# Optimization experiments

Measured on AMD Instinct MI355X. Metric: run time of the kernel, lower is better.

Reference implementation:

```python
import jax, jax.numpy as jnp
import numpy as np

N = 100000   # nodes
E = 1600000  # edges
D = 128      # in_dim == hidden_dim
EL = 100000  # label edges for decode


def setup_inputs() -> dict:
    key = jax.random.key(0)
    k1, k2, k3, k4, k5 = jax.random.split(key, 5)
    x = jax.random.normal(k1, (N, D), dtype=jnp.float32)
    edge_index = jax.random.randint(k2, (2, E), 0, N, dtype=jnp.int64)
    edge_label_index = jax.random.randint(k3, (2, EL), 0, N, dtype=jnp.int64)
    # Glorot-ish init for GCN weights
    scale = 1.0 / np.sqrt(D)
    W1 = jax.random.normal(k4, (D, D), dtype=jnp.float32) * scale
    W2 = jax.random.normal(k5, (D, D), dtype=jnp.float32) * scale
    b1 = jnp.zeros((D,), dtype=jnp.float32)
    b2 = jnp.zeros((D,), dtype=jnp.float32)
    return {"x": x, "edge_index": edge_index, "edge_label_index": edge_label_index,
            "W1": W1, "b1": b1, "W2": W2, "b2": b2}


def gcn_conv(x, src, dst, W, b, num_nodes):
    # PyG GCNConv: add self-loops, symmetric D^-1/2 A D^-1/2 normalization
    loop = jnp.arange(num_nodes, dtype=src.dtype)
    s = jnp.concatenate([src, loop])
    d = jnp.concatenate([dst, loop])
    deg = jax.ops.segment_sum(jnp.ones(d.shape, dtype=x.dtype), d, num_segments=num_nodes)
    dinv = jnp.where(deg > 0, jax.lax.rsqrt(jnp.maximum(deg, 1.0)), 0.0)
    norm = dinv[s] * dinv[d]                      # [E+N]
    h = x @ W                                     # [N, H]
    msg = h[s] * norm[:, None]                    # gather + scale
    out = jax.ops.segment_sum(msg, d, num_segments=num_nodes)  # scatter-add
    return out + b


def reference(x, edge_index, edge_label_index, W1, b1, W2, b2):
    src, dst = edge_index[0], edge_index[1]
    z = jax.nn.relu(gcn_conv(x, src, dst, W1, b1, N))
    z = jax.nn.relu(gcn_conv(z, src, dst, W2, b2, N))
    # decode: edge-wise dot product
    s, d = edge_label_index[0], edge_label_index[1]
    return jnp.sum(z[s] * z[d], axis=-1)          # [EL]
```

## Files before the change

### kernel.cpp

```cpp
#include <hip/hip_runtime.h>
#include <hip/hip_bf16.h>
#include <hip/hip_fp16.h>


typedef _Float16 half8 __attribute__((ext_vector_type(8)));
typedef float floatx4 __attribute__((ext_vector_type(4)));

#define BK_SHIFT 8
#define BSC_EDGES 2048
#define SLAB_CAP 5120
#define WPAD 136

__global__ __launch_bounds__(128) void k_wprep(const float* __restrict__ W1,
                                               const float* __restrict__ W2,
                                               _Float16* __restrict__ WT1,
                                               _Float16* __restrict__ WT2,
                                               int* __restrict__ bfill) {
    int b = blockIdx.x;
    const float* W = (b < 128) ? W1 : W2;
    _Float16* WT = (b < 128) ? WT1 : WT2;
    int k = b & 127;
    int c = threadIdx.x;
    WT[c * 128 + k] = (_Float16)W[k * 128 + c];
    if (b < 4) bfill[b * 128 + c] = 0;
}

__global__ __launch_bounds__(256) void k_bscatter(const int* __restrict__ src,
                                                  const int* __restrict__ dst,
                                                  int* __restrict__ bfill,
                                                  int2* __restrict__ pairs,
                                                  int E, int nbk) {
    __shared__ int lcnt[1024];
    __shared__ int delta[1024];
    __shared__ int ssum[256];
    __shared__ int2 stage[BSC_EDGES];
    int tid = threadIdx.x;
    int e0 = blockIdx.x * BSC_EDGES;
    int nloc = E - e0; if (nloc > BSC_EDGES) nloc = BSC_EDGES;

    for (int b = tid; b < nbk; b += 256) lcnt[b] = 0;
    __syncthreads();

    int d[BSC_EDGES / 256], s[BSC_EDGES / 256];
#pragma unroll
    for (int k = 0; k < BSC_EDGES / 256; ++k) {
        int e = e0 + k * 256 + tid;
        if (e < E) {
            d[k] = dst[e];
            s[k] = src[e];
            atomicAdd(&lcnt[d[k] >> BK_SHIFT], 1);
        } else d[k] = -1;
    }
    __syncthreads();

    const int gpb = (nbk + 255) >> 8;
    int c[4], mysum = 0;
    for (int t = 0; t < gpb; ++t) {
        int b = tid * gpb + t;
        c[t] = (b < nbk) ? lcnt[b] : 0;
        mysum += c[t];
    }
    ssum[tid] = mysum;
    __syncthreads();
    for (int off = 1; off < 256; off <<= 1) {
        int t = (tid >= off) ? ssum[tid - off] : 0;
        __syncthreads();
        ssum[tid] += t;
        __syncthreads();
    }
    int base = ssum[tid] - mysum;
    for (int t = 0; t < gpb; ++t) {
        int b = tid * gpb + t;
        if (b < nbk) {
            int g = c[t] ? atomicAdd(&bfill[b], c[t]) : 0;
            delta[b] = b * SLAB_CAP + g - base;
            lcnt[b] = base;
            base += c[t];
        }
    }
    __syncthreads();

#pragma unroll
    for (int k = 0; k < BSC_EDGES / 256; ++k) {
        if (d[k] >= 0) {
            int b = d[k] >> BK_SHIFT;
            int lp = atomicAdd(&lcnt[b], 1);
            int2 p; p.x = s[k]; p.y = d[k];
            stage[lp] = p;
        }
    }
    __syncthreads();

    for (int j = tid; j < nloc; j += 256) {
        int2 p = stage[j];
        pairs[delta[p.y >> BK_SHIFT] + j] = p;
    }
}

__global__ __launch_bounds__(256) void k_csr(const int2* __restrict__ pairs,
                                             const int* __restrict__ bfill,
                                             int* __restrict__ row_start,
                                             int* __restrict__ cnt,
                                             float* __restrict__ dinv,
                                             int* __restrict__ srcs, int n) {
    __shared__ int lcnt[256];
    __shared__ int lpos[256];
    int tid = threadIdx.x;
    int b = blockIdx.x;
    lcnt[tid] = 0;
    __syncthreads();
    int beg = b * SLAB_CAP, end = beg + bfill[b];
    for (int i = beg + tid; i < end; i += 256)
        atomicAdd(&lcnt[pairs[i].y & 255], 1);
    __syncthreads();
    int c = lcnt[tid];
    lpos[tid] = c;
    __syncthreads();
    for (int off = 1; off < 256; off <<= 1) {
        int t = (tid >= off) ? lpos[tid - off] : 0;
        __syncthreads();
        lpos[tid] += t;
        __syncthreads();
    }
    int rs = beg + lpos[tid] - c;
    int v = (b << BK_SHIFT) + tid;
    if (v < n) {
        row_start[v] = rs;
        cnt[v] = c;
        dinv[v] = rsqrtf((float)c + 1.0f);
    }
    __syncthreads();
    lpos[tid] = rs;
    __syncthreads();
    for (int i = beg + tid; i < end; i += 256) {
        int2 p = pairs[i];
        int loc = atomicAdd(&lpos[p.y & 255], 1);
        srcs[loc] = p.x;
    }
}

template <typename AT>
__global__ __launch_bounds__(256) void k_gemm_mfma(const AT* __restrict__ X,
                                                   const _Float16* __restrict__ WT,
                                                   const float* __restrict__ dinv,
                                                   _Float16* __restrict__ G, int n) {
    __shared__ _Float16 Wl[128 * WPAD];
    int tid = threadIdx.x;
    {
        const half8* w8 = (const half8*)WT;
#pragma unroll
        for (int i = 0; i < 8; ++i) {
            int idx = i * 256 + tid;
            int r = idx >> 4, cc = idx & 15;
            *(half8*)(Wl + r * WPAD + cc * 8) = w8[idx];
        }
    }
    __syncthreads();

    auto loadA = [](const AT* p) -> half8 {
        if constexpr (sizeof(AT) == 4) {
            const float4* f = (const float4*)p;
            float4 f0 = f[0], f1 = f[1];
            half8 a;
            a[0] = (_Float16)f0.x; a[1] = (_Float16)f0.y;
            a[2] = (_Float16)f0.z; a[3] = (_Float16)f0.w;
            a[4] = (_Float16)f1.x; a[5] = (_Float16)f1.y;
            a[6] = (_Float16)f1.z; a[7] = (_Float16)f1.w;
            return a;
        } else {
            return *(const half8*)p;
        }
    };

    int wave = tid >> 6, lane = tid & 63;
    int q = lane >> 4, ln = lane & 15;
    int m0 = blockIdx.x * 128 + wave * 32;
    int mA0 = m0 + ln;      if (mA0 >= n) mA0 = n - 1;
    int mA1 = m0 + 16 + ln; if (mA1 >= n) mA1 = n - 1;
    const AT* xr0 = X + (size_t)mA0 * 128;
    const AT* xr1 = X + (size_t)mA1 * 128;

    floatx4 acc[2][8];
#pragma unroll
    for (int p = 0; p < 2; ++p)
#pragma unroll
        for (int t = 0; t < 8; ++t) acc[p][t] = (floatx4){0.f, 0.f, 0.f, 0.f};

#pragma unroll
    for (int kc = 0; kc < 128; kc += 32) {
        half8 a0 = loadA(xr0 + kc + q * 8);
        half8 a1 = loadA(xr1 + kc + q * 8);
#pragma unroll
        for (int t = 0; t < 8; ++t) {
            half8 b = *(const half8*)(Wl + (size_t)(t * 16 + ln) * WPAD + kc + q * 8);
            acc[0][t] = __builtin_amdgcn_mfma_f32_16x16x32_f16(a0, b, acc[0][t], 0, 0, 0);
            acc[1][t] = __builtin_amdgcn_mfma_f32_16x16x32_f16(a1, b, acc[1][t], 0, 0, 0);
        }
    }

#pragma unroll
    for (int p = 0; p < 2; ++p) {
#pragma unroll
        for (int r = 0; r < 4; ++r) {
            int row = m0 + p * 16 + q * 4 + r;
            if (row < n) {
                float dv = dinv[row];
                _Float16* grow = G + (size_t)row * 128 + ln;
#pragma unroll
                for (int t = 0; t < 8; ++t)
                    grow[t * 16] = (_Float16)(acc[p][t][r] * dv);
            }
        }
    }
}

__global__ __launch_bounds__(256) void k_gather_relu(const _Float16* __restrict__ G,
                                                     const int* __restrict__ srcs,
                                                     const int* __restrict__ row_start,
                                                     const int* __restrict__ cnt,
                                                     const float* __restrict__ dinv,
                                                     const float* __restrict__ bias,
                                                     _Float16* __restrict__ Z, int n) {
    int v = blockIdx.x * 16 + (threadIdx.x >> 4);
    int lane = threadIdx.x & 15;
    if (v >= n) return;
    const half8* G8 = (const half8*)G;

    half8 self = G8[(size_t)v * 16 + lane];
    float acc[8], acc2[8];
#pragma unroll
    for (int j = 0; j < 8; ++j) { acc[j] = (float)self[j]; acc2[j] = 0.f; }

    int beg = row_start[v], deg = cnt[v];
    int e = 0;
    for (; e + 3 < deg; e += 4) {
        int s0 = srcs[beg + e];
        int s1 = srcs[beg + e + 1];
        int s2 = srcs[beg + e + 2];
        int s3 = srcs[beg + e + 3];
        half8 t0 = G8[(size_t)s0 * 16 + lane];
        half8 t1 = G8[(size_t)s1 * 16 + lane];
        half8 t2 = G8[(size_t)s2 * 16 + lane];
        half8 t3 = G8[(size_t)s3 * 16 + lane];
#pragma unroll
        for (int j = 0; j < 8; ++j) {
            acc[j]  += (float)t0[j] + (float)t1[j];
            acc2[j] += (float)t2[j] + (float)t3[j];
        }
    }
    for (; e < deg; ++e) {
        int s0 = srcs[beg + e];
        half8 t0 = G8[(size_t)s0 * 16 + lane];
#pragma unroll
        for (int j = 0; j < 8; ++j) acc[j] += (float)t0[j];
    }

    float dv = dinv[v];
    const float4* b4 = (const float4*)bias;
    float4 bb0 = b4[lane * 2], bb1 = b4[lane * 2 + 1];
    float bf[8] = {bb0.x, bb0.y, bb0.z, bb0.w, bb1.x, bb1.y, bb1.z, bb1.w};
    half8 zo;
#pragma unroll
    for (int j = 0; j < 8; ++j) {
        float z = dv * (acc[j] + acc2[j]) + bf[j];
        zo[j] = (_Float16)fmaxf(z, 0.f);
    }
    ((half8*)Z)[(size_t)v * 16 + lane] = zo;
}

__global__ __launch_bounds__(256) void k_decode(const _Float16* __restrict__ Z,
                                                const int* __restrict__ eli,
                                                float* __restrict__ out, int el) {
    int sub = threadIdx.x >> 4, lane = threadIdx.x & 15;
    int e = blockIdx.x * 16 + sub;
    if (e >= el) return;
    int s = eli[e], d = eli[el + e];
    const half8* Z8 = (const half8*)Z;
    half8 a = Z8[(size_t)s * 16 + lane];
    half8 b = Z8[(size_t)d * 16 + lane];
    float dot = 0.f;
#pragma unroll
    for (int j = 0; j < 8; ++j) dot += (float)a[j] * (float)b[j];
#pragma unroll
    for (int off = 8; off; off >>= 1) dot += __shfl_down(dot, off, 16);
    if (lane == 0) out[e] = dot;
}

extern "C" void kernel_launch(void* const* d_in, const int* in_sizes, int n_in,
                              void* d_out, int out_size, void* d_ws, size_t ws_size,
                              hipStream_t stream) {
    const float* x  = (const float*)d_in[0];
    const int*  ei  = (const int*)d_in[1];
    const int*  eli = (const int*)d_in[2];
    const float* W1 = (const float*)d_in[3];
    const float* b1 = (const float*)d_in[4];
    const float* W2 = (const float*)d_in[5];
    const float* b2 = (const float*)d_in[6];
    float* out = (float*)d_out;

    const int N  = in_sizes[0] / 128;
    const int E  = in_sizes[1] / 2;
    const int EL = in_sizes[2] / 2;
    const int* src = ei;
    const int* dst = ei + E;
    const int NBK = (N + 255) >> BK_SHIFT;

    char* ws = (char*)d_ws;
    size_t off = 0;
    auto alloc = [&](size_t bytes) -> void* {
        void* p = ws + off;
        off += bytes;
        off = (off + 255) & ~(size_t)255;
        return p;
    };
    int*       cnt       = (int*)alloc((size_t)N * 4);
    int*       row_start = (int*)alloc((size_t)N * 4);
    float*     dinv      = (float*)alloc((size_t)N * 4);
    int*       bfill     = (int*)alloc(4096);
    _Float16*  WT1       = (_Float16*)alloc(128 * 128 * 2);
    _Float16*  WT2       = (_Float16*)alloc(128 * 128 * 2);
    int*       srcs      = (int*)alloc((size_t)NBK * SLAB_CAP * 4);
    int2*      pairs     = (int2*)alloc((size_t)NBK * SLAB_CAP * 8);
    _Float16*  buf0      = (_Float16*)alloc((size_t)N * 128 * 2);
    _Float16*  buf1      = (_Float16*)alloc((size_t)N * 128 * 2);

    k_wprep<<<256, 128, 0, stream>>>(W1, W2, WT1, WT2, bfill);

    k_bscatter<<<(E + BSC_EDGES - 1) / BSC_EDGES, 256, 0, stream>>>(src, dst, bfill, pairs, E, NBK);
    k_csr<<<NBK, 256, 0, stream>>>(pairs, bfill, row_start, cnt, dinv, srcs, N);

    k_gemm_mfma<float><<<(N + 127) / 128, 256, 0, stream>>>(x, WT1, dinv, buf0, N);
    k_gather_relu<<<(N + 15) / 16, 256, 0, stream>>>(buf0, srcs, row_start, cnt, dinv, b1, buf1, N);
    k_gemm_mfma<_Float16><<<(N + 127) / 128, 256, 0, stream>>>(buf1, WT2, dinv, buf0, N);
    k_gather_relu<<<(N + 15) / 16, 256, 0, stream>>>(buf0, srcs, row_start, cnt, dinv, b2, buf1, N);
    k_decode<<<(EL + 15) / 16, 256, 0, stream>>>(buf1, eli, out, EL);
}
```

Measured before the change: 307.7 us.

## Store node features as column-sliced planes to localize gather working set

```diff
diff --git a/kernel.cpp b/kernel.cpp
--- a/kernel.cpp
+++ b/kernel.cpp
@@ -10,6 +10,7 @@
 #define BSC_EDGES 2048
 #define SLAB_CAP 5120
 #define WPAD 136
+#define NSLICE 8
 
 __global__ __launch_bounds__(128) void k_wprep(const float* __restrict__ W1,
                                                const float* __restrict__ W2,
@@ -157,19 +158,17 @@
     }
     __syncthreads();
 
+    const size_t pl = (size_t)n * 16;
+
     auto loadA = [](const AT* p) -> half8 {
-        if constexpr (sizeof(AT) == 4) {
-            const float4* f = (const float4*)p;
-            float4 f0 = f[0], f1 = f[1];
-            half8 a;
-            a[0] = (_Float16)f0.x; a[1] = (_Float16)f0.y;
-            a[2] = (_Float16)f0.z; a[3] = (_Float16)f0.w;
-            a[4] = (_Float16)f1.x; a[5] = (_Float16)f1.y;
-            a[6] = (_Float16)f1.z; a[7] = (_Float16)f1.w;
-            return a;
-        } else {
-            return *(const half8*)p;
-        }
+        const float4* f = (const float4*)p;
+        float4 f0 = f[0], f1 = f[1];
+        half8 a;
+        a[0] = (_Float16)f0.x; a[1] = (_Float16)f0.y;
+        a[2] = (_Float16)f0.z; a[3] = (_Float16)f0.w;
+        a[4] = (_Float16)f1.x; a[5] = (_Float16)f1.y;
+        a[6] = (_Float16)f1.z; a[7] = (_Float16)f1.w;
+        return a;
     };
 
     int wave = tid >> 6, lane = tid & 63;
@@ -188,8 +187,16 @@
 
 #pragma unroll
     for (int kc = 0; kc < 128; kc += 32) {
-        half8 a0 = loadA(xr0 + kc + q * 8);
-        half8 a1 = loadA(xr1 + kc + q * 8);
+        half8 a0, a1;
+        if constexpr (sizeof(AT) == 4) {
+            a0 = loadA(xr0 + kc + q * 8);
+            a1 = loadA(xr1 + kc + q * 8);
+        } else {
+            int col0 = kc + q * 8;
+            const _Float16* base = (const _Float16*)X + (size_t)(col0 >> 4) * pl + (col0 & 15);
+            a0 = *(const half8*)(base + (size_t)mA0 * 16);
+            a1 = *(const half8*)(base + (size_t)mA1 * 16);
+        }
 #pragma unroll
         for (int t = 0; t < 8; ++t) {
             half8 b = *(const half8*)(Wl + (size_t)(t * 16 + ln) * WPAD + kc + q * 8);
@@ -205,10 +212,10 @@
             int row = m0 + p * 16 + q * 4 + r;
             if (row < n) {
                 float dv = dinv[row];
-                _Float16* grow = G + (size_t)row * 128 + ln;
+                _Float16* grow = G + (size_t)row * 16 + ln;
 #pragma unroll
                 for (int t = 0; t < 8; ++t)
-                    grow[t * 16] = (_Float16)(acc[p][t][r] * dv);
+                    grow[t * pl] = (_Float16)(acc[p][t][r] * dv);
             }
         }
     }
@@ -221,12 +228,14 @@
                                                      const float* __restrict__ dinv,
                                                      const float* __restrict__ bias,
                                                      _Float16* __restrict__ Z, int n) {
-    int v = blockIdx.x * 16 + (threadIdx.x >> 4);
-    int lane = threadIdx.x & 15;
+    int slice = blockIdx.x & 7;
+    int v = (blockIdx.x >> 3) * 128 + (threadIdx.x >> 1);
     if (v >= n) return;
-    const half8* G8 = (const half8*)G;
-
-    half8 self = G8[(size_t)v * 16 + lane];
+    int h = threadIdx.x & 1;
+    size_t pl8 = (size_t)n * 2;
+    const half8* Gp = (const half8*)G + (size_t)slice * pl8;
+
+    half8 self = Gp[(size_t)v * 2 + h];
     float acc[8], acc2[8];
 #pragma unroll
     for (int j = 0; j < 8; ++j) { acc[j] = (float)self[j]; acc2[j] = 0.f; }
@@ -234,14 +243,14 @@
     int beg = row_start[v], deg = cnt[v];
     int e = 0;
     for (; e + 3 < deg; e += 4) {
-        int s0 = srcs[beg + e];
-        int s1 = srcs[beg + e + 1];
-        int s2 = srcs[beg + e + 2];
-        int s3 = srcs[beg + e + 3];
-        half8 t0 = G8[(size_t)s0 * 16 + lane];
-        half8 t1 = G8[(size_t)s1 * 16 + lane];
-        half8 t2 = G8[(size_t)s2 * 16 + lane];
-        half8 t3 = G8[(size_t)s3 * 16 + lane];
+        int s0 = __builtin_nontemporal_load(srcs + beg + e);
+        int s1 = __builtin_nontemporal_load(srcs + beg + e + 1);
+        int s2 = __builtin_nontemporal_load(srcs + beg + e + 2);
+        int s3 = __builtin_nontemporal_load(srcs + beg + e + 3);
+        half8 t0 = Gp[(size_t)s0 * 2 + h];
+        half8 t1 = Gp[(size_t)s1 * 2 + h];
+        half8 t2 = Gp[(size_t)s2 * 2 + h];
+        half8 t3 = Gp[(size_t)s3 * 2 + h];
 #pragma unroll
         for (int j = 0; j < 8; ++j) {
             acc[j]  += (float)t0[j] + (float)t1[j];
@@ -249,15 +258,15 @@
         }
     }
     for (; e < deg; ++e) {
-        int s0 = srcs[beg + e];
-        half8 t0 = G8[(size_t)s0 * 16 + lane];
+        int s0 = __builtin_nontemporal_load(srcs + beg + e);
+        half8 t0 = Gp[(size_t)s0 * 2 + h];
 #pragma unroll
         for (int j = 0; j < 8; ++j) acc[j] += (float)t0[j];
     }
 
     float dv = dinv[v];
     const float4* b4 = (const float4*)bias;
-    float4 bb0 = b4[lane * 2], bb1 = b4[lane * 2 + 1];
+    float4 bb0 = b4[slice * 4 + h * 2], bb1 = b4[slice * 4 + h * 2 + 1];
     float bf[8] = {bb0.x, bb0.y, bb0.z, bb0.w, bb1.x, bb1.y, bb1.z, bb1.w};
     half8 zo;
 #pragma unroll
@@ -265,19 +274,21 @@
         float z = dv * (acc[j] + acc2[j]) + bf[j];
         zo[j] = (_Float16)fmaxf(z, 0.f);
     }
-    ((half8*)Z)[(size_t)v * 16 + lane] = zo;
+    ((half8*)Z)[(size_t)slice * pl8 + (size_t)v * 2 + h] = zo;
 }
 
 __global__ __launch_bounds__(256) void k_decode(const _Float16* __restrict__ Z,
                                                 const int* __restrict__ eli,
-                                                float* __restrict__ out, int el) {
+                                                float* __restrict__ out, int el, int n) {
     int sub = threadIdx.x >> 4, lane = threadIdx.x & 15;
     int e = blockIdx.x * 16 + sub;
     if (e >= el) return;
     int s = eli[e], d = eli[el + e];
-    const half8* Z8 = (const half8*)Z;
-    half8 a = Z8[(size_t)s * 16 + lane];
-    half8 b = Z8[(size_t)d * 16 + lane];
+    size_t pl8 = (size_t)n * 2;
+    const half8* Zp = (const half8*)Z + (size_t)(lane >> 1) * pl8;
+    int h = lane & 1;
+    half8 a = Zp[(size_t)s * 2 + h];
+    half8 b = Zp[(size_t)d * 2 + h];
     float dot = 0.f;
 #pragma unroll
     for (int j = 0; j < 8; ++j) dot += (float)a[j] * (float)b[j];
@@ -329,9 +340,10 @@
     k_bscatter<<<(E + BSC_EDGES - 1) / BSC_EDGES, 256, 0, stream>>>(src, dst, bfill, pairs, E, NBK);
     k_csr<<<NBK, 256, 0, stream>>>(pairs, bfill, row_start, cnt, dinv, srcs, N);
 
+    const int GRID_GATHER = ((N + 127) / 128) * NSLICE;
     k_gemm_mfma<float><<<(N + 127) / 128, 256, 0, stream>>>(x, WT1, dinv, buf0, N);
-    k_gather_relu<<<(N + 15) / 16, 256, 0, stream>>>(buf0, srcs, row_start, cnt, dinv, b1, buf1, N);
+    k_gather_relu<<<GRID_GATHER, 256, 0, stream>>>(buf0, srcs, row_start, cnt, dinv, b1, buf1, N);
     k_gemm_mfma<_Float16><<<(N + 127) / 128, 256, 0, stream>>>(buf1, WT2, dinv, buf0, N);
-    k_gather_relu<<<(N + 15) / 16, 256, 0, stream>>>(buf0, srcs, row_start, cnt, dinv, b2, buf1, N);
-    k_decode<<<(EL + 15) / 16, 256, 0, stream>>>(buf1, eli, out, EL);
-}
+    k_gather_relu<<<GRID_GATHER, 256, 0, stream>>>(buf0, srcs, row_start, cnt, dinv, b2, buf1, N);
+    k_decode<<<(EL + 15) / 16, 256, 0, stream>>>(buf1, eli, out, EL, N);
+}
```

New measurement: 464.1 us. 50.8% more time.

## Fuse CSR build with first GEMM and move source normalization into gather

Applied to the files above, without the earlier changes.

```diff
diff --git a/kernel.cpp b/kernel.cpp
--- a/kernel.cpp
+++ b/kernel.cpp
@@ -97,55 +97,58 @@
     }
 }
 
-__global__ __launch_bounds__(256) void k_csr(const int2* __restrict__ pairs,
-                                             const int* __restrict__ bfill,
-                                             int* __restrict__ row_start,
-                                             int* __restrict__ cnt,
-                                             float* __restrict__ dinv,
-                                             int* __restrict__ srcs, int n) {
-    __shared__ int lcnt[256];
-    __shared__ int lpos[256];
+template <typename AT>
+__global__ __launch_bounds__(256) void k_csr_gemm(const int2* __restrict__ pairs,
+                                                  const int* __restrict__ bfill,
+                                                  int* __restrict__ row_start,
+                                                  int* __restrict__ cnt,
+                                                  float* __restrict__ dinv,
+                                                  int* __restrict__ srcs,
+                                                  const AT* __restrict__ X,
+                                                  const _Float16* __restrict__ WT,
+                                                  _Float16* __restrict__ G,
+                                                  int n, int nbk) {
+    __shared__ __align__(16) char smem[128 * WPAD * 2];
     int tid = threadIdx.x;
-    int b = blockIdx.x;
-    lcnt[tid] = 0;
-    __syncthreads();
-    int beg = b * SLAB_CAP, end = beg + bfill[b];
-    for (int i = beg + tid; i < end; i += 256)
-        atomicAdd(&lcnt[pairs[i].y & 255], 1);
-    __syncthreads();
-    int c = lcnt[tid];
-    lpos[tid] = c;
-    __syncthreads();
-    for (int off = 1; off < 256; off <<= 1) {
-        int t = (tid >= off) ? lpos[tid - off] : 0;
-        __syncthreads();
-        lpos[tid] += t;
-        __syncthreads();
-    }
-    int rs = beg + lpos[tid] - c;
-    int v = (b << BK_SHIFT) + tid;
-    if (v < n) {
-        row_start[v] = rs;
-        cnt[v] = c;
-        dinv[v] = rsqrtf((float)c + 1.0f);
-    }
-    __syncthreads();
-    lpos[tid] = rs;
-    __syncthreads();
-    for (int i = beg + tid; i < end; i += 256) {
-        int2 p = pairs[i];
-        int loc = atomicAdd(&lpos[p.y & 255], 1);
-        srcs[loc] = p.x;
-    }
-}
-
-template <typename AT>
-__global__ __launch_bounds__(256) void k_gemm_mfma(const AT* __restrict__ X,
-                                                   const _Float16* __restrict__ WT,
-                                                   const float* __restrict__ dinv,
-                                                   _Float16* __restrict__ G, int n) {
-    __shared__ _Float16 Wl[128 * WPAD];
-    int tid = threadIdx.x;
+
+    if ((int)blockIdx.x < nbk) {
+        int* lcnt = (int*)smem;
+        int* lpos = lcnt + 256;
+        int b = blockIdx.x;
+        lcnt[tid] = 0;
+        __syncthreads();
+        int beg = b * SLAB_CAP, end = beg + bfill[b];
+        for (int i = beg + tid; i < end; i += 256)
+            atomicAdd(&lcnt[pairs[i].y & 255], 1);
+        __syncthreads();
+        int c = lcnt[tid];
+        lpos[tid] = c;
+        __syncthreads();
+        for (int off = 1; off < 256; off <<= 1) {
+            int t = (tid >= off) ? lpos[tid - off] : 0;
+            __syncthreads();
+            lpos[tid] += t;
+            __syncthreads();
+        }
+        int rs = beg + lpos[tid] - c;
+        int v = (b << BK_SHIFT) + tid;
+        if (v < n) {
+            row_start[v] = rs;
+            cnt[v] = c;
+            dinv[v] = rsqrtf((float)c + 1.0f);
+        }
+        __syncthreads();
+        lpos[tid] = rs;
+        __syncthreads();
+        for (int i = beg + tid; i < end; i += 256) {
+            int2 p = pairs[i];
+            int loc = atomicAdd(&lpos[p.y & 255], 1);
+            srcs[loc] = p.x;
+        }
+        return;
+    }
+
+    _Float16* Wl = (_Float16*)smem;
     {
         const half8* w8 = (const half8*)WT;
 #pragma unroll
@@ -172,6 +175,80 @@
         }
     };
 
+    int bid = blockIdx.x - nbk;
+    int wave = tid >> 6, lane = tid & 63;
+    int q = lane >> 4, ln = lane & 15;
+    int m0 = bid * 128 + wave * 32;
+    int mA0 = m0 + ln;      if (mA0 >= n) mA0 = n - 1;
+    int mA1 = m0 + 16 + ln; if (mA1 >= n) mA1 = n - 1;
+    const AT* xr0 = X + (size_t)mA0 * 128;
+    const AT* xr1 = X + (size_t)mA1 * 128;
+
+    floatx4 acc[2][8];
+#pragma unroll
+    for (int p = 0; p < 2; ++p)
+#pragma unroll
+        for (int t = 0; t < 8; ++t) acc[p][t] = (floatx4){0.f, 0.f, 0.f, 0.f};
+
+#pragma unroll
+    for (int kc = 0; kc < 128; kc += 32) {
+        half8 a0 = loadA(xr0 + kc + q * 8);
+        half8 a1 = loadA(xr1 + kc + q * 8);
+#pragma unroll
+        for (int t = 0; t < 8; ++t) {
+            half8 b = *(const half8*)(Wl + (size_t)(t * 16 + ln) * WPAD + kc + q * 8);
+            acc[0][t] = __builtin_amdgcn_mfma_f32_16x16x32_f16(a0, b, acc[0][t], 0, 0, 0);
+            acc[1][t] = __builtin_amdgcn_mfma_f32_16x16x32_f16(a1, b, acc[1][t], 0, 0, 0);
+        }
+    }
+
+#pragma unroll
+    for (int p = 0; p < 2; ++p) {
+#pragma unroll
+        for (int r = 0; r < 4; ++r) {
+            int row = m0 + p * 16 + q * 4 + r;
+            if (row < n) {
+                _Float16* grow = G + (size_t)row * 128 + ln;
+#pragma unroll
+                for (int t = 0; t < 8; ++t)
+                    grow[t * 16] = (_Float16)acc[p][t][r];
+            }
+        }
+    }
+}
+
+template <typename AT>
+__global__ __launch_bounds__(256) void k_gemm_mfma(const AT* __restrict__ X,
+                                                   const _Float16* __restrict__ WT,
+                                                   _Float16* __restrict__ G, int n) {
+    __shared__ _Float16 Wl[128 * WPAD];
+    int tid = threadIdx.x;
+    {
+        const half8* w8 = (const half8*)WT;
+#pragma unroll
+        for (int i = 0; i < 8; ++i) {
+            int idx = i * 256 + tid;
+            int r = idx >> 4, cc = idx & 15;
+            *(half8*)(Wl + r * WPAD + cc * 8) = w8[idx];
+        }
+    }
+    __syncthreads();
+
+    auto loadA = [](const AT* p) -> half8 {
+        if constexpr (sizeof(AT) == 4) {
+            const float4* f = (const float4*)p;
+            float4 f0 = f[0], f1 = f[1];
+            half8 a;
+            a[0] = (_Float16)f0.x; a[1] = (_Float16)f0.y;
+            a[2] = (_Float16)f0.z; a[3] = (_Float16)f0.w;
+            a[4] = (_Float16)f1.x; a[5] = (_Float16)f1.y;
+            a[6] = (_Float16)f1.z; a[7] = (_Float16)f1.w;
+            return a;
+        } else {
+            return *(const half8*)p;
+        }
+    };
+
     int wave = tid >> 6, lane = tid & 63;
     int q = lane >> 4, ln = lane & 15;
     int m0 = blockIdx.x * 128 + wave * 32;
@@ -204,11 +281,10 @@
         for (int r = 0; r < 4; ++r) {
             int row = m0 + p * 16 + q * 4 + r;
             if (row < n) {
-                float dv = dinv[row];
                 _Float16* grow = G + (size_t)row * 128 + ln;
 #pragma unroll
                 for (int t = 0; t < 8; ++t)
-                    grow[t * 16] = (_Float16)(acc[p][t][r] * dv);
+                    grow[t * 16] = (_Float16)acc[p][t][r];
             }
         }
     }
@@ -226,10 +302,11 @@
     if (v >= n) return;
     const half8* G8 = (const half8*)G;
 
+    float dv = dinv[v];
     half8 self = G8[(size_t)v * 16 + lane];
     float acc[8], acc2[8];
 #pragma unroll
-    for (int j = 0; j < 8; ++j) { acc[j] = (float)self[j]; acc2[j] = 0.f; }
+    for (int j = 0; j < 8; ++j) { acc[j] = dv * (float)self[j]; acc2[j] = 0.f; }
 
     int beg = row_start[v], deg = cnt[v];
     int e = 0;
@@ -238,24 +315,28 @@
         int s1 = srcs[beg + e + 1];
         int s2 = srcs[beg + e + 2];
         int s3 = srcs[beg + e + 3];
+        float d0 = dinv[s0];
+        float d1 = dinv[s1];
+        float d2 = dinv[s2];
+        float d3 = dinv[s3];
         half8 t0 = G8[(size_t)s0 * 16 + lane];
         half8 t1 = G8[(size_t)s1 * 16 + lane];
         half8 t2 = G8[(size_t)s2 * 16 + lane];
         half8 t3 = G8[(size_t)s3 * 16 + lane];
 #pragma unroll
         for (int j = 0; j < 8; ++j) {
-            acc[j]  += (float)t0[j] + (float)t1[j];
-            acc2[j] += (float)t2[j] + (float)t3[j];
+            acc[j]  += d0 * (float)t0[j] + d1 * (float)t1[j];
+            acc2[j] += d2 * (float)t2[j] + d3 * (float)t3[j];
         }
     }
     for (; e < deg; ++e) {
         int s0 = srcs[beg + e];
+        float d0 = dinv[s0];
         half8 t0 = G8[(size_t)s0 * 16 + lane];
 #pragma unroll
-        for (int j = 0; j < 8; ++j) acc[j] += (float)t0[j];
-    }
-
-    float dv = dinv[v];
+        for (int j = 0; j < 8; ++j) acc[j] += d0 * (float)t0[j];
+    }
+
     const float4* b4 = (const float4*)bias;
     float4 bb0 = b4[lane * 2], bb1 = b4[lane * 2 + 1];
     float bf[8] = {bb0.x, bb0.y, bb0.z, bb0.w, bb1.x, bb1.y, bb1.z, bb1.w};
@@ -304,6 +385,7 @@
     const int* src = ei;
     const int* dst = ei + E;
     const int NBK = (N + 255) >> BK_SHIFT;
+    const int GB  = (N + 127) / 128;
 
     char* ws = (char*)d_ws;
     size_t off = 0;
@@ -327,11 +409,12 @@
     k_wprep<<<256, 128, 0, stream>>>(W1, W2, WT1, WT2, bfill);
 
     k_bscatter<<<(E + BSC_EDGES - 1) / BSC_EDGES, 256, 0, stream>>>(src, dst, bfill, pairs, E, NBK);
-    k_csr<<<NBK, 256, 0, stream>>>(pairs, bfill, row_start, cnt, dinv, srcs, N);
-
-    k_gemm_mfma<float><<<(N + 127) / 128, 256, 0, stream>>>(x, WT1, dinv, buf0, N);
+
+    k_csr_gemm<float><<<NBK + GB, 256, 0, stream>>>(pairs, bfill, row_start, cnt, dinv,
+                                                    srcs, x, WT1, buf0, N, NBK);
+
     k_gather_relu<<<(N + 15) / 16, 256, 0, stream>>>(buf0, srcs, row_start, cnt, dinv, b1, buf1, N);
-    k_gemm_mfma<_Float16><<<(N + 127) / 128, 256, 0, stream>>>(buf1, WT2, dinv, buf0, N);
+    k_gemm_mfma<_Float16><<<GB, 256, 0, stream>>>(buf1, WT2, buf0, N);
     k_gather_relu<<<(N + 15) / 16, 256, 0, stream>>>(buf0, srcs, row_start, cnt, dinv, b2, buf1, N);
     k_decode<<<(EL + 15) / 16, 256, 0, stream>>>(buf1, eli, out, EL);
 }
```

Measured after the change: 307.6 us. Within noise of the previous version (-0.0%).
